# Performance work log

Measured on AMD Instinct MI355X. Metric: run time of the kernel, lower is better.

Reference implementation:

```python
import jax, jax.numpy as jnp
import numpy as np

N = 100000       # num nodes
E = 3200000      # num edges (avg degree 32)
F_IN = 128       # num_node_features
HID = 16         # hidden dim hard-coded in Net
C = 10           # num_classes


def setup_inputs() -> dict:
    key = jax.random.key(0)
    k1, k2, k3, k4 = jax.random.split(key, 4)
    x = jax.random.normal(k1, (N, F_IN), dtype=jnp.float32)
    edge_index = jax.random.randint(k2, (2, E), 0, N, dtype=jnp.int32)
    W1 = jax.random.normal(k3, (F_IN, HID), dtype=jnp.float32) * 0.05
    b1 = jnp.zeros((HID,), dtype=jnp.float32)
    W2 = jax.random.normal(k4, (HID, C), dtype=jnp.float32) * 0.05
    b2 = jnp.zeros((C,), dtype=jnp.float32)
    return {"x": x, "edge_index": edge_index, "W1": W1, "b1": b1, "W2": W2, "b2": b2}


def reference(x, edge_index, W1, b1, W2, b2):
    # GCNConv: out = D^{-1/2} (A + I) D^{-1/2} X W + b   (add self-loops)
    loops = jnp.arange(N, dtype=edge_index.dtype)
    row = jnp.concatenate([edge_index[0], loops])  # source nodes
    col = jnp.concatenate([edge_index[1], loops])  # target nodes

    # symmetric normalization (degrees include self-loops, so deg >= 1)
    deg = jax.ops.segment_sum(jnp.ones_like(col, dtype=jnp.float32), col, num_segments=N)
    dis = jax.lax.rsqrt(deg)
    norm = dis[row] * dis[col]  # [E+N]

    def gcn_conv(h, W, b):
        h = h @ W                               # [N, d_out] small GEMM first
        msg = h[row] * norm[:, None]            # gather + scale, [E+N, d_out]
        out = jax.ops.segment_sum(msg, col, num_segments=N)  # scatter-add
        return out + b

    h = jax.nn.relu(gcn_conv(x, W1, b1))
    # F.dropout(training=False) is identity in eval mode
    logits = gcn_conv(h, W2, b2)
    return jax.nn.log_softmax(logits, axis=1)
```

## Files before the change

kernel.cpp:

```cpp
#include <hip/hip_runtime.h>
#include <math.h>

#define N_NODES 100000
#define N_EDGES 3200000
#define F_IN 128
#define HID 16
#define C_OUT 10
#define WIN 256
#define NDIG 391
#define PNB2 512
#define EPB 6250
#define SCN (NDIG * PNB2)
#define SB1 782
#define MAXE 40

typedef unsigned short u16;
typedef unsigned int u32;

__device__ __forceinline__ float bf2f(u16 u) {
    return __uint_as_float(((u32)u) << 16);
}
__device__ __forceinline__ u16 f2bf(float f) {
    u32 x = __float_as_uint(f);
    u32 r = (x + 0x7fffu + ((x >> 16) & 1u)) >> 16;
    return (u16)r;
}

__global__ void k_pcnt(const int* __restrict__ col, int* __restrict__ blkhistA) {
    __shared__ int h[NDIG];
    for (int i = threadIdx.x; i < NDIG; i += 256) h[i] = 0;
    __syncthreads();
    int lo = blockIdx.x * EPB, hi = lo + EPB;
    for (int e = lo + threadIdx.x; e < hi; e += 256)
        atomicAdd(&h[col[e] >> 8], 1);
    __syncthreads();
    for (int d = threadIdx.x; d < NDIG; d += 256)
        blkhistA[d * PNB2 + blockIdx.x] = h[d];
}

__global__ void k_s1(const int* __restrict__ blkhistA, int* __restrict__ psum) {
    __shared__ int sm[256];
    int i = blockIdx.x * 256 + threadIdx.x;
    sm[threadIdx.x] = blkhistA[i];
    __syncthreads();
    for (int off = 128; off > 0; off >>= 1) {
        if (threadIdx.x < off) sm[threadIdx.x] += sm[threadIdx.x + off];
        __syncthreads();
    }
    if (threadIdx.x == 0) psum[blockIdx.x] = sm[0];
}

__global__ void k_s2(int* __restrict__ psum) {
    const int T = 1024;
    __shared__ int part[T];
    int t = threadIdx.x;
    int v0 = (t < SB1) ? psum[t] : 0;
    part[t] = v0;
    __syncthreads();
    for (int off = 1; off < T; off <<= 1) {
        int v = part[t];
        int u = (t >= off) ? part[t - off] : 0;
        __syncthreads();
        part[t] = v + u;
        __syncthreads();
    }
    if (t < SB1) psum[t] = part[t] - v0;
}

__global__ void k_s3(const int* __restrict__ blkhistA, const int* __restrict__ psum,
                     int* __restrict__ blkhistB) {
    __shared__ int sm[256];
    int i = blockIdx.x * 256 + threadIdx.x;
    int t = threadIdx.x;
    int v = blkhistA[i];
    sm[t] = v;
    __syncthreads();
    for (int off = 1; off < 256; off <<= 1) {
        int a = sm[t];
        int b = (t >= off) ? sm[t - off] : 0;
        __syncthreads();
        sm[t] = a + b;
        __syncthreads();
    }
    blkhistB[i] = psum[blockIdx.x] + sm[t] - v;
}

__global__ void k_pwrite(const int* __restrict__ row, const int* __restrict__ col,
                         const int* __restrict__ blkhistA, const int* __restrict__ blkhistB,
                         u32* __restrict__ staging) {
    __shared__ u32 sorted[EPB];
    __shared__ u16 dwin[EPB];
    __shared__ int gbase[NDIG];
    __shared__ int lbase[NDIG];
    __shared__ int lcur[NDIG];
    __shared__ int scan[512];

    int t = threadIdx.x;
    int b = blockIdx.x;
    int hv = 0;
    if (t < NDIG) {
        hv = blkhistA[t * PNB2 + b];
        gbase[t] = blkhistB[t * PNB2 + b];
        lcur[t] = 0;
    }
    scan[t] = hv;
    __syncthreads();
    for (int off = 1; off < 512; off <<= 1) {
        int v = scan[t];
        int u = (t >= off) ? scan[t - off] : 0;
        __syncthreads();
        scan[t] = v + u;
        __syncthreads();
    }
    if (t < NDIG) lbase[t] = scan[t] - hv;
    __syncthreads();

    int lo = b * EPB, hi = lo + EPB;
    for (int e = lo + t; e < hi; e += 512) {
        int c = col[e];
        int d = c >> 8;
        int rank = atomicAdd(&lcur[d], 1);
        int pos = lbase[d] + rank;
        sorted[pos] = ((u32)(c & 255) << 17) | (u32)row[e];
        dwin[pos] = (u16)d;
    }
    __syncthreads();

    for (int i = t; i < EPB; i += 512) {
        int d = dwin[i];
        staging[gbase[d] + (i - lbase[d])] = sorted[i];
    }
}

__global__ void k_csr(u32* staging, const int* __restrict__ blkhistB,
                      int* __restrict__ offs, float* __restrict__ dis) {
    __shared__ int cnt[WIN];
    __shared__ int base[WIN];
    int w = blockIdx.x;
    int t = threadIdx.x;
    cnt[t] = 0;
    __syncthreads();
    int start = blkhistB[w * PNB2];
    int end = (w == NDIG - 1) ? N_EDGES : blkhistB[(w + 1) * PNB2];
    u32 buf[MAXE];
    int n = 0;
#pragma unroll
    for (int k = 0; k < MAXE; k++) {
        int i = start + k * 256 + t;
        if (i < end) {
            u32 e = staging[i];
            buf[k] = e;
            n = k + 1;
            atomicAdd(&cnt[e >> 17], 1);
        }
    }
    __syncthreads();
    base[t] = cnt[t];
    __syncthreads();
    for (int off = 1; off < WIN; off <<= 1) {
        int v = base[t];
        int u = (t >= off) ? base[t - off] : 0;
        __syncthreads();
        base[t] = v + u;
        __syncthreads();
    }
    int excl = base[t] - cnt[t];
    base[t] = excl;
    int node = w * WIN + t;
    if (node < N_NODES) {
        offs[node] = start + excl;
        dis[node] = rsqrtf(1.0f + (float)cnt[t]);
    }
    if (w == 0 && t == 0) offs[N_NODES] = N_EDGES;
    __syncthreads();
    cnt[t] = 0;
    __syncthreads();
#pragma unroll
    for (int k = 0; k < MAXE; k++) {
        if (k < n) {
            u32 e = buf[k];
            int cl = (int)(e >> 17);
            int rank = atomicAdd(&cnt[cl], 1);
            staging[start + base[cl] + rank] = e;
        }
    }
}

__global__ void k_gemm1(const float* __restrict__ x, const float* __restrict__ W1,
                        const float* __restrict__ dis, u16* __restrict__ h1s) {
    __shared__ float Ws[F_IN * HID];
    for (int t = threadIdx.x; t < F_IN * HID; t += blockDim.x) Ws[t] = W1[t];
    __syncthreads();

    int node = blockIdx.x * blockDim.x + threadIdx.x;
    if (node >= N_NODES) return;

    float acc[HID];
#pragma unroll
    for (int j = 0; j < HID; j++) acc[j] = 0.f;

    const float4* xr = (const float4*)(x + (size_t)node * F_IN);
#pragma unroll 2
    for (int k4 = 0; k4 < F_IN / 4; k4++) {
        float4 v = xr[k4];
        float xv[4] = {v.x, v.y, v.z, v.w};
#pragma unroll
        for (int kk = 0; kk < 4; kk++) {
            const float4* wr = (const float4*)(Ws + (k4 * 4 + kk) * HID);
            float4 w0 = wr[0], w1 = wr[1], w2 = wr[2], w3 = wr[3];
            float xs = xv[kk];
            acc[0]  += xs * w0.x; acc[1]  += xs * w0.y; acc[2]  += xs * w0.z; acc[3]  += xs * w0.w;
            acc[4]  += xs * w1.x; acc[5]  += xs * w1.y; acc[6]  += xs * w1.z; acc[7]  += xs * w1.w;
            acc[8]  += xs * w2.x; acc[9]  += xs * w2.y; acc[10] += xs * w2.z; acc[11] += xs * w2.w;
            acc[12] += xs * w3.x; acc[13] += xs * w3.y; acc[14] += xs * w3.z; acc[15] += xs * w3.w;
        }
    }

    float d = dis[node];
    u32 p[8];
#pragma unroll
    for (int i = 0; i < 8; i++)
        p[i] = (u32)f2bf(acc[2 * i] * d) | ((u32)f2bf(acc[2 * i + 1] * d) << 16);
    u32* dst = (u32*)(h1s + (size_t)node * HID);
#pragma unroll
    for (int i = 0; i < 8; i++) dst[i] = p[i];
}

__global__ void k_gather1(const int* __restrict__ offs, const u32* __restrict__ csr,
                          const float* __restrict__ dis, const u16* __restrict__ h1s,
                          u16* __restrict__ agg1) {
    int t = blockIdx.x * 256 + threadIdx.x;
    int node = t >> 3;
    int f2 = t & 7;
    const u32* hb = (const u32*)h1s;
    u32 v = hb[(size_t)node * 8 + f2];
    float a0 = bf2f((u16)(v & 0xffff));
    float a1 = bf2f((u16)(v >> 16));
    int s0 = offs[node], s1 = offs[node + 1];
    int j = s0;
    for (; j < s1 && (j & 3); j++) {
        int s = (int)(csr[j] & 0x1FFFFu);
        u32 w = hb[(size_t)s * 8 + f2];
        a0 += bf2f((u16)(w & 0xffff));
        a1 += bf2f((u16)(w >> 16));
    }
    for (; j + 4 <= s1; j += 4) {
        uint4 ss = *(const uint4*)(csr + j);
        u32 w0 = hb[(size_t)(ss.x & 0x1FFFFu) * 8 + f2];
        u32 w1 = hb[(size_t)(ss.y & 0x1FFFFu) * 8 + f2];
        u32 w2 = hb[(size_t)(ss.z & 0x1FFFFu) * 8 + f2];
        u32 w3 = hb[(size_t)(ss.w & 0x1FFFFu) * 8 + f2];
        a0 += bf2f((u16)(w0 & 0xffff)); a1 += bf2f((u16)(w0 >> 16));
        a0 += bf2f((u16)(w1 & 0xffff)); a1 += bf2f((u16)(w1 >> 16));
        a0 += bf2f((u16)(w2 & 0xffff)); a1 += bf2f((u16)(w2 >> 16));
        a0 += bf2f((u16)(w3 & 0xffff)); a1 += bf2f((u16)(w3 >> 16));
    }
    for (; j < s1; j++) {
        int s = (int)(csr[j] & 0x1FFFFu);
        u32 w = hb[(size_t)s * 8 + f2];
        a0 += bf2f((u16)(w & 0xffff));
        a1 += bf2f((u16)(w >> 16));
    }
    float dc = dis[node];
    ((u32*)agg1)[(size_t)node * 8 + f2] =
        (u32)f2bf(a0 * dc) | ((u32)f2bf(a1 * dc) << 16);
}

__global__ void k_layer2(const u16* __restrict__ agg1, const float* __restrict__ b1,
                         const float* __restrict__ W2, const float* __restrict__ dis,
                         u16* __restrict__ h2s) {
    __shared__ float Ws[HID * C_OUT];
    __shared__ float b1s[HID];
    if (threadIdx.x < HID * C_OUT) Ws[threadIdx.x] = W2[threadIdx.x];
    if (threadIdx.x < HID) b1s[threadIdx.x] = b1[threadIdx.x];
    __syncthreads();

    int node = blockIdx.x * blockDim.x + threadIdx.x;
    if (node >= N_NODES) return;

    const uint4* ar = (const uint4*)(agg1 + (size_t)node * HID);
    uint4 q0 = ar[0], q1 = ar[1];
    u32 qs[8] = {q0.x, q0.y, q0.z, q0.w, q1.x, q1.y, q1.z, q1.w};

    float acc[C_OUT];
#pragma unroll
    for (int k = 0; k < C_OUT; k++) acc[k] = 0.f;

#pragma unroll
    for (int i = 0; i < 8; i++) {
        u32 q = qs[i];
        float v0 = bf2f((u16)(q & 0xffff));
        float v1 = bf2f((u16)(q >> 16));
        int j0 = 2 * i, j1 = 2 * i + 1;
        float h0 = fmaxf(v0 + b1s[j0], 0.f);
        float h1v = fmaxf(v1 + b1s[j1], 0.f);
#pragma unroll
        for (int k = 0; k < C_OUT; k++) acc[k] += h0 * Ws[j0 * C_OUT + k] + h1v * Ws[j1 * C_OUT + k];
    }

    float d = dis[node];
    u32 p[8];
#pragma unroll
    for (int i = 0; i < 5; i++)
        p[i] = (u32)f2bf(acc[2 * i] * d) | ((u32)f2bf(acc[2 * i + 1] * d) << 16);
    p[5] = 0; p[6] = 0; p[7] = 0;
    u32* dst = (u32*)(h2s + (size_t)node * HID);
#pragma unroll
    for (int i = 0; i < 8; i++) dst[i] = p[i];
}

__global__ void k_gather2(const int* __restrict__ offs, const u32* __restrict__ csr,
                          const float* __restrict__ dis, const u16* __restrict__ h2s,
                          float* __restrict__ agg2) {
    int t = blockIdx.x * 256 + threadIdx.x;
    int node = t >> 3;
    int f2 = t & 7;
    if (f2 >= 5) return;
    const u32* hb = (const u32*)h2s;
    u32 v = hb[(size_t)node * 8 + f2];
    float a0 = bf2f((u16)(v & 0xffff));
    float a1 = bf2f((u16)(v >> 16));
    int s0 = offs[node], s1 = offs[node + 1];
    int j = s0;
    for (; j < s1 && (j & 3); j++) {
        int s = (int)(csr[j] & 0x1FFFFu);
        u32 w = hb[(size_t)s * 8 + f2];
        a0 += bf2f((u16)(w & 0xffff));
        a1 += bf2f((u16)(w >> 16));
    }
    for (; j + 4 <= s1; j += 4) {
        uint4 ss = *(const uint4*)(csr + j);
        u32 w0 = hb[(size_t)(ss.x & 0x1FFFFu) * 8 + f2];
        u32 w1 = hb[(size_t)(ss.y & 0x1FFFFu) * 8 + f2];
        u32 w2 = hb[(size_t)(ss.z & 0x1FFFFu) * 8 + f2];
        u32 w3 = hb[(size_t)(ss.w & 0x1FFFFu) * 8 + f2];
        a0 += bf2f((u16)(w0 & 0xffff)); a1 += bf2f((u16)(w0 >> 16));
        a0 += bf2f((u16)(w1 & 0xffff)); a1 += bf2f((u16)(w1 >> 16));
        a0 += bf2f((u16)(w2 & 0xffff)); a1 += bf2f((u16)(w2 >> 16));
        a0 += bf2f((u16)(w3 & 0xffff)); a1 += bf2f((u16)(w3 >> 16));
    }
    for (; j < s1; j++) {
        int s = (int)(csr[j] & 0x1FFFFu);
        u32 w = hb[(size_t)s * 8 + f2];
        a0 += bf2f((u16)(w & 0xffff));
        a1 += bf2f((u16)(w >> 16));
    }
    float dc = dis[node];
    float2 o = make_float2(a0 * dc, a1 * dc);
    *(float2*)(agg2 + (size_t)node * C_OUT + 2 * f2) = o;
}

__global__ void k_final(float* __restrict__ agg2, const float* __restrict__ b2) {
    __shared__ float b2s[C_OUT];
    if (threadIdx.x < C_OUT) b2s[threadIdx.x] = b2[threadIdx.x];
    __syncthreads();

    int i = blockIdx.x * blockDim.x + threadIdx.x;
    if (i >= N_NODES) return;

    float* ar = agg2 + (size_t)i * C_OUT;
    float v[C_OUT];
    float m = -1e30f;
#pragma unroll
    for (int k = 0; k < C_OUT; k++) {
        v[k] = ar[k] + b2s[k];
        m = fmaxf(m, v[k]);
    }
    float s = 0.f;
#pragma unroll
    for (int k = 0; k < C_OUT; k++) s += expf(v[k] - m);
    float ls = logf(s) + m;
#pragma unroll
    for (int k = 0; k < C_OUT; k++) ar[k] = v[k] - ls;
}

extern "C" void kernel_launch(void* const* d_in, const int* in_sizes, int n_in,
                              void* d_out, int out_size, void* d_ws, size_t ws_size,
                              hipStream_t stream) {
    const float* x  = (const float*)d_in[0];
    const int*   ei = (const int*)d_in[1];
    const float* W1 = (const float*)d_in[2];
    const float* b1 = (const float*)d_in[3];
    const float* W2 = (const float*)d_in[4];
    const float* b2 = (const float*)d_in[5];
    float* out = (float*)d_out;

    const int* row = ei;
    const int* col = ei + N_EDGES;

    char* ws = (char*)d_ws;
    float* dis      = (float*)(ws);
    int*   offs     = (int*)(ws + 400000);
    int*   blkhistA = (int*)(ws + 800016);
    int*   blkhistB = (int*)(ws + 1600784);
    int*   psum     = (int*)(ws + 2401552);
    u32*   staging  = (u32*)(ws + 2404688);
    u16*   h1s      = (u16*)(ws + 15204688);
    u16*   h2s      = (u16*)(ws + 15204688);
    u16*   agg1     = (u16*)d_out;
    float* agg2     = out;

    const int B = 256;
    int gN  = (N_NODES + B - 1) / B;
    int gN8 = (N_NODES * 8) / B;

    k_pcnt  <<<PNB2, B, 0, stream>>>(col, blkhistA);
    k_s1    <<<SB1, B, 0, stream>>>(blkhistA, psum);
    k_s2    <<<1, 1024, 0, stream>>>(psum);
    k_s3    <<<SB1, B, 0, stream>>>(blkhistA, psum, blkhistB);
    k_pwrite<<<PNB2, 512, 0, stream>>>(row, col, blkhistA, blkhistB, staging);
    k_csr   <<<NDIG, B, 0, stream>>>(staging, blkhistB, offs, dis);
    k_gemm1 <<<gN, B, 0, stream>>>(x, W1, dis, h1s);
    k_gather1<<<gN8, B, 0, stream>>>(offs, staging, dis, h1s, agg1);
    k_layer2<<<gN, B, 0, stream>>>(agg1, b1, W2, dis, h2s);
    k_gather2<<<gN8, B, 0, stream>>>(offs, staging, dis, h2s, agg2);
    k_final <<<gN, B, 0, stream>>>(agg2, b2);
}
```

Baseline: 251.3 us.

## Vectorize edge loads, widen gather to 16-byte rows, fuse log-softmax into gather2

Changes the partition to 500 blocks of 6400 edges so that each block's edge slice is 16-byte aligned, then reads col/row as uint4 in the histogram and scatter kernels. Both gather kernels now use 2 threads per node, each loading a full uint4 (8 bf16 values) per neighbour instead of 8 threads each loading one u32. This cuts redundant CSR index reads and issues fewer, wider memory requests. The final bias plus log-softmax is fused into gather2 using a lane shuffle, which removes the k_final launch and its round trip of agg2 through memory. The cost is less thread parallelism per node in the latency-bound gathers.

```diff
diff --git a/kernel.cpp b/kernel.cpp
--- a/kernel.cpp
+++ b/kernel.cpp
@@ -8,10 +8,10 @@
 #define C_OUT 10
 #define WIN 256
 #define NDIG 391
-#define PNB2 512
-#define EPB 6250
+#define PNB2 500
+#define EPB 6400
 #define SCN (NDIG * PNB2)
-#define SB1 782
+#define SB1 764
 #define MAXE 40
 
 typedef unsigned short u16;
@@ -25,14 +25,25 @@
     u32 r = (x + 0x7fffu + ((x >> 16) & 1u)) >> 16;
     return (u16)r;
 }
+__device__ __forceinline__ void acc8(float* a, uint4 w) {
+    a[0] += bf2f((u16)(w.x & 0xffff)); a[1] += bf2f((u16)(w.x >> 16));
+    a[2] += bf2f((u16)(w.y & 0xffff)); a[3] += bf2f((u16)(w.y >> 16));
+    a[4] += bf2f((u16)(w.z & 0xffff)); a[5] += bf2f((u16)(w.z >> 16));
+    a[6] += bf2f((u16)(w.w & 0xffff)); a[7] += bf2f((u16)(w.w >> 16));
+}
 
 __global__ void k_pcnt(const int* __restrict__ col, int* __restrict__ blkhistA) {
     __shared__ int h[NDIG];
     for (int i = threadIdx.x; i < NDIG; i += 256) h[i] = 0;
     __syncthreads();
-    int lo = blockIdx.x * EPB, hi = lo + EPB;
-    for (int e = lo + threadIdx.x; e < hi; e += 256)
-        atomicAdd(&h[col[e] >> 8], 1);
+    const uint4* c4 = (const uint4*)(col + blockIdx.x * EPB);
+    for (int i = threadIdx.x; i < EPB / 4; i += 256) {
+        uint4 c = c4[i];
+        atomicAdd(&h[c.x >> 8], 1);
+        atomicAdd(&h[c.y >> 8], 1);
+        atomicAdd(&h[c.z >> 8], 1);
+        atomicAdd(&h[c.w >> 8], 1);
+    }
     __syncthreads();
     for (int d = threadIdx.x; d < NDIG; d += 256)
         blkhistA[d * PNB2 + blockIdx.x] = h[d];
@@ -41,7 +52,7 @@
 __global__ void k_s1(const int* __restrict__ blkhistA, int* __restrict__ psum) {
     __shared__ int sm[256];
     int i = blockIdx.x * 256 + threadIdx.x;
-    sm[threadIdx.x] = blkhistA[i];
+    sm[threadIdx.x] = (i < SCN) ? blkhistA[i] : 0;
     __syncthreads();
     for (int off = 128; off > 0; off >>= 1) {
         if (threadIdx.x < off) sm[threadIdx.x] += sm[threadIdx.x + off];
@@ -72,7 +83,7 @@
     __shared__ int sm[256];
     int i = blockIdx.x * 256 + threadIdx.x;
     int t = threadIdx.x;
-    int v = blkhistA[i];
+    int v = (i < SCN) ? blkhistA[i] : 0;
     sm[t] = v;
     __syncthreads();
     for (int off = 1; off < 256; off <<= 1) {
@@ -82,12 +93,13 @@
         sm[t] = a + b;
         __syncthreads();
     }
-    blkhistB[i] = psum[blockIdx.x] + sm[t] - v;
-}
-
-__global__ void k_pwrite(const int* __restrict__ row, const int* __restrict__ col,
-                         const int* __restrict__ blkhistA, const int* __restrict__ blkhistB,
-                         u32* __restrict__ staging) {
+    if (i < SCN) blkhistB[i] = psum[blockIdx.x] + sm[t] - v;
+}
+
+__global__ void __launch_bounds__(512) k_pwrite(
+        const int* __restrict__ row, const int* __restrict__ col,
+        const int* __restrict__ blkhistA, const int* __restrict__ blkhistB,
+        u32* __restrict__ staging) {
     __shared__ u32 sorted[EPB];
     __shared__ u16 dwin[EPB];
     __shared__ int gbase[NDIG];
@@ -115,14 +127,20 @@
     if (t < NDIG) lbase[t] = scan[t] - hv;
     __syncthreads();
 
-    int lo = b * EPB, hi = lo + EPB;
-    for (int e = lo + t; e < hi; e += 512) {
-        int c = col[e];
-        int d = c >> 8;
-        int rank = atomicAdd(&lcur[d], 1);
-        int pos = lbase[d] + rank;
-        sorted[pos] = ((u32)(c & 255) << 17) | (u32)row[e];
-        dwin[pos] = (u16)d;
+    const uint4* c4 = (const uint4*)(col + b * EPB);
+    const uint4* r4 = (const uint4*)(row + b * EPB);
+    for (int i = t; i < EPB / 4; i += 512) {
+        uint4 c = c4[i];
+        uint4 r = r4[i];
+        int d, rank, pos;
+        d = (int)(c.x >> 8); rank = atomicAdd(&lcur[d], 1); pos = lbase[d] + rank;
+        sorted[pos] = ((c.x & 255u) << 17) | r.x; dwin[pos] = (u16)d;
+        d = (int)(c.y >> 8); rank = atomicAdd(&lcur[d], 1); pos = lbase[d] + rank;
+        sorted[pos] = ((c.y & 255u) << 17) | r.y; dwin[pos] = (u16)d;
+        d = (int)(c.z >> 8); rank = atomicAdd(&lcur[d], 1); pos = lbase[d] + rank;
+        sorted[pos] = ((c.z & 255u) << 17) | r.z; dwin[pos] = (u16)d;
+        d = (int)(c.w >> 8); rank = atomicAdd(&lcur[d], 1); pos = lbase[d] + rank;
+        sorted[pos] = ((c.w & 255u) << 17) | r.w; dwin[pos] = (u16)d;
     }
     __syncthreads();
 
@@ -230,40 +248,33 @@
                           const float* __restrict__ dis, const u16* __restrict__ h1s,
                           u16* __restrict__ agg1) {
     int t = blockIdx.x * 256 + threadIdx.x;
-    int node = t >> 3;
-    int f2 = t & 7;
-    const u32* hb = (const u32*)h1s;
-    u32 v = hb[(size_t)node * 8 + f2];
-    float a0 = bf2f((u16)(v & 0xffff));
-    float a1 = bf2f((u16)(v >> 16));
+    if (t >= N_NODES * 2) return;
+    int node = t >> 1;
+    int half = t & 1;
+    const uint4* hb = (const uint4*)h1s;
+    float a[8] = {0.f, 0.f, 0.f, 0.f, 0.f, 0.f, 0.f, 0.f};
+    acc8(a, hb[(size_t)node * 2 + half]);
     int s0 = offs[node], s1 = offs[node + 1];
     int j = s0;
-    for (; j < s1 && (j & 3); j++) {
-        int s = (int)(csr[j] & 0x1FFFFu);
-        u32 w = hb[(size_t)s * 8 + f2];
-        a0 += bf2f((u16)(w & 0xffff));
-        a1 += bf2f((u16)(w >> 16));
-    }
+    for (; j < s1 && (j & 3); j++)
+        acc8(a, hb[(size_t)(csr[j] & 0x1FFFFu) * 2 + half]);
     for (; j + 4 <= s1; j += 4) {
         uint4 ss = *(const uint4*)(csr + j);
-        u32 w0 = hb[(size_t)(ss.x & 0x1FFFFu) * 8 + f2];
-        u32 w1 = hb[(size_t)(ss.y & 0x1FFFFu) * 8 + f2];
-        u32 w2 = hb[(size_t)(ss.z & 0x1FFFFu) * 8 + f2];
-        u32 w3 = hb[(size_t)(ss.w & 0x1FFFFu) * 8 + f2];
-        a0 += bf2f((u16)(w0 & 0xffff)); a1 += bf2f((u16)(w0 >> 16));
-        a0 += bf2f((u16)(w1 & 0xffff)); a1 += bf2f((u16)(w1 >> 16));
-        a0 += bf2f((u16)(w2 & 0xffff)); a1 += bf2f((u16)(w2 >> 16));
-        a0 += bf2f((u16)(w3 & 0xffff)); a1 += bf2f((u16)(w3 >> 16));
-    }
-    for (; j < s1; j++) {
-        int s = (int)(csr[j] & 0x1FFFFu);
-        u32 w = hb[(size_t)s * 8 + f2];
-        a0 += bf2f((u16)(w & 0xffff));
-        a1 += bf2f((u16)(w >> 16));
-    }
+        uint4 w0 = hb[(size_t)(ss.x & 0x1FFFFu) * 2 + half];
+        uint4 w1 = hb[(size_t)(ss.y & 0x1FFFFu) * 2 + half];
+        uint4 w2 = hb[(size_t)(ss.z & 0x1FFFFu) * 2 + half];
+        uint4 w3 = hb[(size_t)(ss.w & 0x1FFFFu) * 2 + half];
+        acc8(a, w0); acc8(a, w1); acc8(a, w2); acc8(a, w3);
+    }
+    for (; j < s1; j++)
+        acc8(a, hb[(size_t)(csr[j] & 0x1FFFFu) * 2 + half]);
     float dc = dis[node];
-    ((u32*)agg1)[(size_t)node * 8 + f2] =
-        (u32)f2bf(a0 * dc) | ((u32)f2bf(a1 * dc) << 16);
+    uint4 o;
+    o.x = (u32)f2bf(a[0] * dc) | ((u32)f2bf(a[1] * dc) << 16);
+    o.y = (u32)f2bf(a[2] * dc) | ((u32)f2bf(a[3] * dc) << 16);
+    o.z = (u32)f2bf(a[4] * dc) | ((u32)f2bf(a[5] * dc) << 16);
+    o.w = (u32)f2bf(a[6] * dc) | ((u32)f2bf(a[7] * dc) << 16);
+    ((uint4*)agg1)[(size_t)node * 2 + half] = o;
 }
 
 __global__ void k_layer2(const u16* __restrict__ agg1, const float* __restrict__ b1,
@@ -311,67 +322,57 @@
 
 __global__ void k_gather2(const int* __restrict__ offs, const u32* __restrict__ csr,
                           const float* __restrict__ dis, const u16* __restrict__ h2s,
-                          float* __restrict__ agg2) {
+                          const float* __restrict__ b2, float* __restrict__ out) {
+    __shared__ float b2s[C_OUT];
+    if (threadIdx.x < C_OUT) b2s[threadIdx.x] = b2[threadIdx.x];
+    __syncthreads();
+
     int t = blockIdx.x * 256 + threadIdx.x;
-    int node = t >> 3;
-    int f2 = t & 7;
-    if (f2 >= 5) return;
-    const u32* hb = (const u32*)h2s;
-    u32 v = hb[(size_t)node * 8 + f2];
-    float a0 = bf2f((u16)(v & 0xffff));
-    float a1 = bf2f((u16)(v >> 16));
+    if (t >= N_NODES * 2) return;
+    int node = t >> 1;
+    int half = t & 1;
+    const uint4* hb = (const uint4*)h2s;
+    float a[8] = {0.f, 0.f, 0.f, 0.f, 0.f, 0.f, 0.f, 0.f};
+    acc8(a, hb[(size_t)node * 2 + half]);
     int s0 = offs[node], s1 = offs[node + 1];
     int j = s0;
-    for (; j < s1 && (j & 3); j++) {
-        int s = (int)(csr[j] & 0x1FFFFu);
-        u32 w = hb[(size_t)s * 8 + f2];
-        a0 += bf2f((u16)(w & 0xffff));
-        a1 += bf2f((u16)(w >> 16));
-    }
+    for (; j < s1 && (j & 3); j++)
+        acc8(a, hb[(size_t)(csr[j] & 0x1FFFFu) * 2 + half]);
     for (; j + 4 <= s1; j += 4) {
         uint4 ss = *(const uint4*)(csr + j);
-        u32 w0 = hb[(size_t)(ss.x & 0x1FFFFu) * 8 + f2];
-        u32 w1 = hb[(size_t)(ss.y & 0x1FFFFu) * 8 + f2];
-        u32 w2 = hb[(size_t)(ss.z & 0x1FFFFu) * 8 + f2];
-        u32 w3 = hb[(size_t)(ss.w & 0x1FFFFu) * 8 + f2];
-        a0 += bf2f((u16)(w0 & 0xffff)); a1 += bf2f((u16)(w0 >> 16));
-        a0 += bf2f((u16)(w1 & 0xffff)); a1 += bf2f((u16)(w1 >> 16));
-        a0 += bf2f((u16)(w2 & 0xffff)); a1 += bf2f((u16)(w2 >> 16));
-        a0 += bf2f((u16)(w3 & 0xffff)); a1 += bf2f((u16)(w3 >> 16));
-    }
-    for (; j < s1; j++) {
-        int s = (int)(csr[j] & 0x1FFFFu);
-        u32 w = hb[(size_t)s * 8 + f2];
-        a0 += bf2f((u16)(w & 0xffff));
-        a1 += bf2f((u16)(w >> 16));
-    }
+        uint4 w0 = hb[(size_t)(ss.x & 0x1FFFFu) * 2 + half];
+        uint4 w1 = hb[(size_t)(ss.y & 0x1FFFFu) * 2 + half];
+        uint4 w2 = hb[(size_t)(ss.z & 0x1FFFFu) * 2 + half];
+        uint4 w3 = hb[(size_t)(ss.w & 0x1FFFFu) * 2 + half];
+        acc8(a, w0); acc8(a, w1); acc8(a, w2); acc8(a, w3);
+    }
+    for (; j < s1; j++)
+        acc8(a, hb[(size_t)(csr[j] & 0x1FFFFu) * 2 + half]);
+
     float dc = dis[node];
-    float2 o = make_float2(a0 * dc, a1 * dc);
-    *(float2*)(agg2 + (size_t)node * C_OUT + 2 * f2) = o;
-}
-
-__global__ void k_final(float* __restrict__ agg2, const float* __restrict__ b2) {
-    __shared__ float b2s[C_OUT];
-    if (threadIdx.x < C_OUT) b2s[threadIdx.x] = b2[threadIdx.x];
-    __syncthreads();
-
-    int i = blockIdx.x * blockDim.x + threadIdx.x;
-    if (i >= N_NODES) return;
-
-    float* ar = agg2 + (size_t)i * C_OUT;
-    float v[C_OUT];
+    int nf = half ? 2 : 8;
+    float lg[8];
     float m = -1e30f;
 #pragma unroll
-    for (int k = 0; k < C_OUT; k++) {
-        v[k] = ar[k] + b2s[k];
-        m = fmaxf(m, v[k]);
-    }
+    for (int k = 0; k < 8; k++) {
+        lg[k] = a[k] * dc + b2s[(half * 8 + k) % C_OUT];
+        if (k < nf) m = fmaxf(m, lg[k]);
+    }
+    m = fmaxf(m, __shfl_xor(m, 1));
     float s = 0.f;
 #pragma unroll
-    for (int k = 0; k < C_OUT; k++) s += expf(v[k] - m);
+    for (int k = 0; k < 8; k++)
+        if (k < nf) s += expf(lg[k] - m);
+    s += __shfl_xor(s, 1);
     float ls = logf(s) + m;
-#pragma unroll
-    for (int k = 0; k < C_OUT; k++) ar[k] = v[k] - ls;
+    float* dst = out + (size_t)node * C_OUT + half * 8;
+    if (half == 0) {
+#pragma unroll
+        for (int i = 0; i < 4; i++)
+            *(float2*)(dst + 2 * i) = make_float2(lg[2 * i] - ls, lg[2 * i + 1] - ls);
+    } else {
+        *(float2*)dst = make_float2(lg[0] - ls, lg[1] - ls);
+    }
 }
 
 extern "C" void kernel_launch(void* const* d_in, const int* in_sizes, int n_in,
@@ -392,17 +393,17 @@
     float* dis      = (float*)(ws);
     int*   offs     = (int*)(ws + 400000);
     int*   blkhistA = (int*)(ws + 800016);
-    int*   blkhistB = (int*)(ws + 1600784);
-    int*   psum     = (int*)(ws + 2401552);
-    u32*   staging  = (u32*)(ws + 2404688);
-    u16*   h1s      = (u16*)(ws + 15204688);
-    u16*   h2s      = (u16*)(ws + 15204688);
+    int*   blkhistB = (int*)(ws + 1582352);
+    int*   psum     = (int*)(ws + 2364688);
+    u32*   staging  = (u32*)(ws + 2367744);
+    u16*   h1s      = (u16*)(ws + 15167744);
+    u16*   h2s      = (u16*)(ws + 15167744);
     u16*   agg1     = (u16*)d_out;
     float* agg2     = out;
 
     const int B = 256;
     int gN  = (N_NODES + B - 1) / B;
-    int gN8 = (N_NODES * 8) / B;
+    int gN2 = (N_NODES * 2 + B - 1) / B;
 
     k_pcnt  <<<PNB2, B, 0, stream>>>(col, blkhistA);
     k_s1    <<<SB1, B, 0, stream>>>(blkhistA, psum);
@@ -411,8 +412,8 @@
     k_pwrite<<<PNB2, 512, 0, stream>>>(row, col, blkhistA, blkhistB, staging);
     k_csr   <<<NDIG, B, 0, stream>>>(staging, blkhistB, offs, dis);
     k_gemm1 <<<gN, B, 0, stream>>>(x, W1, dis, h1s);
-    k_gather1<<<gN8, B, 0, stream>>>(offs, staging, dis, h1s, agg1);
+    k_gather1<<<gN2, B, 0, stream>>>(offs, staging, dis, h1s, agg1);
     k_layer2<<<gN, B, 0, stream>>>(agg1, b1, W2, dis, h2s);
-    k_gather2<<<gN8, B, 0, stream>>>(offs, staging, dis, h2s, agg2);
-    k_final <<<gN, B, 0, stream>>>(agg2, b2);
-}
+    k_gather2<<<gN2, B, 0, stream>>>(offs, staging, dis, h2s, b2, agg2);
+    (void)agg2;
+}
```

Result: faster. 243.8 us (-3.0%).
